# Performance work log

Measured on AMD Instinct MI355X. Metric: run time of the kernel, lower is better.

The kernel has to match this reference:

```python
import jax, jax.numpy as jnp
import numpy as np

PLAYERS = 8
DMODEL = 256          # cfg.dmodel (per-embedding dim)
DK = 1024             # cfg.dk
WINDOW = 4096         # cfg.window == T here
A_SPACE = 64
DFULL = DMODEL * 2 * PLAYERS   # 4096, the concatenated model dim


def _positional_encoding(T, dmodel):
    # i = 1/10000^(2j/dmodel); pe[:, ::2]=sin(pos*i), pe[:, 1::2]=cos(pos*i)
    i = 1.0 / jnp.power(jnp.float32(10000.0), jnp.arange(0, dmodel, 2, dtype=jnp.float32) / dmodel)
    pos = jnp.arange(T, dtype=jnp.float32)[:, None]
    pe = jnp.zeros((T, dmodel), dtype=jnp.float32)
    pe = pe.at[:, ::2].set(jnp.sin(pos * i))
    pe = pe.at[:, 1::2].set(jnp.cos(pos * i))
    return pe


def setup_inputs() -> dict:
    key = jax.random.key(0)
    ks = jax.random.split(key, 12)
    n_rows = WINDOW * 2 * PLAYERS  # 65536 one-hot rows
    idx = jax.random.randint(ks[0], (n_rows,), 0, PLAYERS + 1)
    obs = jax.nn.one_hot(idx, PLAYERS + 1, dtype=jnp.int32)
    std = 2.0 / (5.0 * DFULL)  # torch.normal(0, var) uses var as std in the source
    return {
        "obs": obs,
        "o_emb": jax.random.normal(ks[1], (PLAYERS + 1, DMODEL), jnp.float32),
        "d_emb": jax.random.normal(ks[2], (PLAYERS + 1, DMODEL), jnp.float32),
        "WQ": jax.random.normal(ks[3], (DFULL, DK), jnp.float32) * std,
        "WK": jax.random.normal(ks[4], (DFULL, DK), jnp.float32) * std,
        "WV": jax.random.normal(ks[5], (DFULL, DK), jnp.float32) * std,
        "WO": jax.random.normal(ks[6], (DK, DK), jnp.float32) * std,
        "Wo_pol": jax.random.normal(ks[7], (A_SPACE, DK), jnp.float32) * 0.02,
        "bo_pol": jnp.zeros((A_SPACE,), jnp.float32),
        "Wd_pol": jax.random.normal(ks[8], (A_SPACE, DK), jnp.float32) * 0.02,
        "bd_pol": jnp.zeros((A_SPACE,), jnp.float32),
        "Wv": jax.random.normal(ks[9], (1, DK), jnp.float32) * 0.02,
        "bv": jnp.zeros((1,), jnp.float32),
    }


def reference(obs, o_emb, d_emb, WQ, WK, WV, WO, Wo_pol, bo_pol, Wd_pol, bd_pol, Wv, bv):
    obs2 = obs.reshape(-1, PLAYERS + 1)
    # torch.where(row == 1)[1] on one-hot rows == argmax
    idx_o = jnp.argmax(obs2[::2], axis=1)   # [T*players]
    idx_d = jnp.argmax(obs2[1::2], axis=1)  # [T*players]
    emb = jnp.concatenate([o_emb[idx_o], d_emb[idx_d]], axis=1)  # [T*players, 2*dmodel]
    x = emb.reshape(-1, DFULL) * jnp.sqrt(jnp.float32(DMODEL))    # [T, DFULL]
    T = x.shape[0]
    x = x + _positional_encoding(T, DFULL)
    q = x @ WQ  # [T, DK]
    k = x @ WK
    v = x @ WV
    att = jax.nn.softmax((q @ k.T) / jnp.sqrt(jnp.float32(DK)), axis=-1)  # [T, T]
    o = (att @ v) @ WO  # [T, DK]
    h = jax.nn.relu(o[-1])  # last position only, [DK]
    o_logits = h @ Wo_pol.T + bo_pol  # [A_SPACE]
    d_logits = h @ Wd_pol.T + bd_pol  # [A_SPACE]
    value = h @ Wv.T + bv             # [1]
    return (o_logits, d_logits, value)
```

## Files before the change

### kernel.cpp

```cpp
#include <hip/hip_runtime.h>
#include <stdint.h>

#define DK      1024
#define NBLK    256
#define NT      1024
#define NBAR    5u
#define LOG2_10000 13.287712379549449f

__device__ __align__(16) float g_e[4096];
__device__ __align__(16) float g_kq[4096];
__device__ __align__(16) float g_ol[1024];
__device__ __align__(16) float g_q8[2][8][1024];
__device__ __align__(16) float g_ctx8[2][8][1024];
__device__ __align__(16) float g_w8[2][8][160];

__device__ unsigned bar_gc[256];
__device__ unsigned bar_gm[32];
__device__ unsigned bar_gen;

__device__ __forceinline__ void stg(float* p, float v) {
    __hip_atomic_store(p, v, __ATOMIC_RELAXED, __HIP_MEMORY_SCOPE_AGENT);
}
__device__ __forceinline__ float lda(const float* p) {
    return __hip_atomic_load(p, __ATOMIC_RELAXED, __HIP_MEMORY_SCOPE_AGENT);
}

__device__ __forceinline__ void gbar_arrive(int bid, unsigned target) {
    asm volatile("s_waitcnt vmcnt(0)" ::: "memory");
    __syncthreads();
    if (threadIdx.x == 0) {
        unsigned g = (unsigned)bid & 7u;
        unsigned old = __hip_atomic_fetch_add(&bar_gc[g * 32], 1u,
                           __ATOMIC_RELAXED, __HIP_MEMORY_SCOPE_AGENT);
        if (old == target * 32u - 1u) {
            unsigned o2 = __hip_atomic_fetch_add(&bar_gm[0], 1u,
                              __ATOMIC_RELAXED, __HIP_MEMORY_SCOPE_AGENT);
            if (o2 == target * 8u - 1u)
                __hip_atomic_store(&bar_gen, target, __ATOMIC_RELEASE,
                                   __HIP_MEMORY_SCOPE_AGENT);
        }
    }
}
__device__ __forceinline__ void gbar_wait(unsigned target) {
    if (threadIdx.x == 0) {
        int gd = 0;
        while (__hip_atomic_load(&bar_gen, __ATOMIC_RELAXED,
                                 __HIP_MEMORY_SCOPE_AGENT) < target) {
            __builtin_amdgcn_s_sleep(1);
            if (++gd > (1 << 17)) break;
        }
    }
    __syncthreads();
}
__device__ __forceinline__ void gbar(int bid, unsigned target) {
    gbar_arrive(bid, target);
    gbar_wait(target);
}

__device__ __forceinline__ float4 bred4(float4 a, float* buf, int tid) {
    #pragma unroll
    for (int off = 32; off; off >>= 1) {
        a.x += __shfl_down(a.x, off, 64);
        a.y += __shfl_down(a.y, off, 64);
        a.z += __shfl_down(a.z, off, 64);
        a.w += __shfl_down(a.w, off, 64);
    }
    float4* b4 = (float4*)buf;
    if ((tid & 63) == 0) b4[tid >> 6] = a;
    __syncthreads();
    float4 r = {0.f, 0.f, 0.f, 0.f};
    if (tid == 0) {
        #pragma unroll
        for (int i = 0; i < 16; ++i) {
            float4 t = b4[i];
            r.x += t.x; r.y += t.y; r.z += t.z; r.w += t.w;
        }
    }
    __syncthreads();
    return r;
}

__global__ __launch_bounds__(1024, 4) void fused_k(
        const int*   __restrict__ obs,
        const float* __restrict__ o_emb,  const float* __restrict__ d_emb,
        const float* __restrict__ WQ,     const float* __restrict__ WK,
        const float* __restrict__ WV,     const float* __restrict__ WO,
        const float* __restrict__ Wo_pol, const float* __restrict__ bo_pol,
        const float* __restrict__ Wd_pol, const float* __restrict__ bd_pol,
        const float* __restrict__ Wv,     const float* __restrict__ bv,
        float* __restrict__ out,          char* __restrict__ ws) {
    (void)ws;

    __shared__ __align__(16) float smem[12416];
    float* axpeL = &smem[12288];
    unsigned char* sidx = (unsigned char*)&smem[12304];
    unsigned* sgen = (unsigned*)&smem[12400];

    int bid = blockIdx.x, tid = threadIdx.x;
    const int w  = ((bid & 7) << 5) | (bid >> 3);
    const int sh = bid & 7;
    const int lane = tid & 63;
    const int ksub = tid >> 8, n4 = tid & 255;

    if (tid == 0)
        *sgen = __hip_atomic_load(&bar_gen, __ATOMIC_RELAXED,
                                  __HIP_MEMORY_SCOPE_AGENT);

    const float4* WQ4 = (const float4*)WQ;
    float4 wqr[4];
    #pragma unroll
    for (int kk = 0; kk < 4; ++kk)
        wqr[kk] = WQ4[(size_t)(w * 16 + ksub * 4 + kk) * 256 + n4];

    int*   lidx = (int*)&smem[4100];
    float* lx   = &smem[4120];
    if (tid < 256) {
        int g = w * 256 + tid;
        const int* r = obs + (size_t)g * 9;
        int id = 0;
        #pragma unroll
        for (int j = 1; j < 9; ++j) id += j * r[j];
        sidx[(tid & ~15) | ((tid & 1) << 3) | ((tid >> 1) & 7)] =
            (unsigned char)id;
    }
    if (tid < 16) {
        const int* rr = obs + (size_t)(65520 + tid) * 9;
        int id2 = 0;
        #pragma unroll
        for (int j = 1; j < 9; ++j) id2 += j * rr[j];
        lidx[(tid & 1) * 8 + (tid >> 1)] = id2;
    }
    __syncthreads();
    const unsigned gen0 = *sgen;
    const int par = (int)((gen0 / NBAR) & 1u);
    float* q8 = &g_q8[par][0][0];
    float* c8 = &g_ctx8[par][0][0];
    float* w8 = &g_w8[par][0][0];
    {
        float* q8n = &g_q8[par ^ 1][0][0];
        float* c8n = &g_ctx8[par ^ 1][0][0];
        float* w8n = &g_w8[par ^ 1][0][0];
        if (tid < 69) {
            int idx = w * 69 + tid;
            if (idx < 8192)       stg(&q8n[idx], 0.0f);
            else if (idx < 16384) stg(&c8n[idx - 8192], 0.0f);
            else if (idx < 17664) stg(&w8n[idx - 16384], 0.0f);
        }
    }
    if (tid < 16) {
        int c = w * 16 + tid;
        int p = c >> 9, rr = c & 511;
        const float* tab = (rr < 256) ? o_emb : d_emb;
        int slot = (rr < 256) ? p : 8 + p;
        int r2 = rr & 255;
        float e = tab[lidx[slot] * 256 + r2];
        float f = exp2f(-((float)(c & ~1) * (1.0f / 4096.0f)) * LOG2_10000);
        float sv, cv;
        __sincosf(4095.0f * f, &sv, &cv);
        lx[tid] = e * 16.0f + ((c & 1) ? cv : sv);
    }
    __syncthreads();
    {
        float4 acc = {0.f, 0.f, 0.f, 0.f};
        #pragma unroll
        for (int kk = 0; kk < 4; ++kk) {
            float xv = lx[ksub * 4 + kk];
            acc.x += xv * wqr[kk].x; acc.y += xv * wqr[kk].y;
            acc.z += xv * wqr[kk].z; acc.w += xv * wqr[kk].w;
        }
        float4* p4 = (float4*)smem;
        p4[ksub * 256 + n4] = acc;
        __syncthreads();
        if (tid < 256) {
            float4 a = p4[tid], b = p4[256 + tid],
                   c2 = p4[512 + tid], d = p4[768 + tid];
            float* dst = &q8[sh * 1024 + tid * 4];
            atomicAdd(dst + 0, a.x + b.x + c2.x + d.x);
            atomicAdd(dst + 1, a.y + b.y + c2.y + d.y);
            atomicAdd(dst + 2, a.z + b.z + c2.z + d.z);
            atomicAdd(dst + 3, a.w + b.w + c2.w + d.w);
        }
    }
    float4 wkr[4];
    gbar_arrive(bid, gen0 + 1);
    {
        const float4* WKr = (const float4*)(WK + (size_t)(w * 16 + (tid >> 6)) * DK);
        #pragma unroll
        for (int i = 0; i < 4; ++i) wkr[i] = WKr[i * 64 + lane];
        float* lemb = &smem[4096];
        float* lfrq = &smem[8724];
        for (int i = tid; i < 2048; i += NT)
            lfrq[i] = exp2f(-((float)(2 * i) * (1.0f / 4096.0f)) * LOG2_10000);
        for (int i = tid; i < 4608; i += NT) {
            int row = i >> 8, r = i & 255;
            lemb[row * 257 + r] = (row < 9) ? o_emb[row * 256 + r]
                                            : d_emb[(row - 9) * 256 + r];
        }
    }
    gbar_wait(gen0 + 1);

    {
        float* qsum = &smem[10772];
        float t = 0.0f;
        #pragma unroll
        for (int s2 = 0; s2 < 8; ++s2) t += lda(&q8[s2 * 1024 + tid]);
        qsum[tid] = t;
        __syncthreads();
        const float4* q4 = (const float4*)qsum;
        float acc = 0.0f;
        #pragma unroll
        for (int i = 0; i < 4; ++i) {
            float4 qq = q4[i * 64 + lane];
            acc += wkr[i].x * qq.x + wkr[i].y * qq.y
                 + wkr[i].z * qq.z + wkr[i].w * qq.w;
        }
        #pragma unroll
        for (int off = 32; off; off >>= 1) acc += __shfl_down(acc, off, 64);
        if (lane == 0) stg(&g_kq[w * 16 + (tid >> 6)], acc * (1.0f / 32.0f));
    }
    gbar(bid, gen0 + 2);

    {
        float* lkq   = smem;
        float* lemb  = &smem[4096];
        float* lfrq  = &smem[8724];
        float* ldot4 = &smem[10772];
        float* le16  = &smem[11360];
        float* lped  = &smem[11380];
        float* lh    = &smem[11400];
        #pragma unroll
        for (int i = 0; i < 4; ++i) {
            int c = tid + NT * i;
            lkq[c] = lda(&g_kq[c]);
        }
        if (tid < 144) lh[tid] = 0.0f;
        __syncthreads();
        if (tid < 576) {
            int p = tid >> 2, q = tid & 3;
            int sg = p / 9, id = p % 9;
            int base = (sg < 8) ? sg * 512 : (sg - 8) * 512 + 256;
            const float* e = lemb + ((sg < 8) ? id : (9 + id)) * 257;
            float a = 0.0f;
            for (int i = 0; i < 64; ++i) {
                int r = q * 64 + ((i + q * 13) & 63);
                a += e[r] * lkq[base + r];
            }
            ldot4[tid] = a;
        }
        {
            int tt = tid >> 6;
            int t = w * 16 + tt;
            float acc = 0.0f;
            #pragma unroll 4
            for (int jj = 0; jj < 32; ++jj) {
                int jf = jj * 64 + lane;
                float f = lfrq[jf];
                float svv, cvv;
                __sincosf((float)t * f, &svv, &cvv);
                acc += svv * lkq[2 * jf] + cvv * lkq[2 * jf + 1];
            }
            #pragma unroll
            for (int off = 32; off; off >>= 1) acc += __shfl_down(acc, off, 64);
            if (lane == 0) lped[tt] = acc;
        }
        __syncthreads();
        if (tid < 16) {
            float tot = lped[tid];
            const uint32_t* ip = (const uint32_t*)(sidx + tid * 16);
            uint32_t u0 = ip[0], u1 = ip[1], u2 = ip[2], u3 = ip[3];
            #pragma unroll
            for (int sg = 0; sg < 16; ++sg) {
                uint32_t u = (sg < 4) ? u0 : (sg < 8) ? u1 : (sg < 12) ? u2 : u3;
                int id = (u >> ((sg & 3) * 8)) & 0xFF;
                int p = (sg * 9 + id) * 4;
                tot += 16.0f * (ldot4[p] + ldot4[p + 1] + ldot4[p + 2] + ldot4[p + 3]);
            }
            float e = expf(tot);
            le16[tid] = e;
            stg(&g_e[w * 16 + tid], e);
        }
        __syncthreads();
        if (tid < 256) {
            int lt = tid >> 4, seg = tid & 15;
            int id = sidx[lt * 16 + seg];
            atomicAdd(&lh[seg * 9 + id], le16[lt]);
        }
        __syncthreads();
        if (tid < 144) atomicAdd(&w8[sh * 160 + tid], lh[tid]);
    }
    float4 wvr[4];
    gbar_arrive(bid, gen0 + 3);
    {
        const float4* WV4 = (const float4*)WV;
        #pragma unroll
        for (int kk = 0; kk < 4; ++kk)
            wvr[kk] = WV4[(size_t)(w * 16 + ksub * 4 + kk) * 256 + n4];
    }
    gbar_wait(gen0 + 3);

    {
        float* leT = smem;
        float* pss = &smem[4352];
        float* psc = &smem[5376];
        float* lw  = &smem[6400];
        float* axv = &smem[6576];
        {
            int c0 = tid * 4, col = tid >> 3;
            float e0 = lda(&g_e[c0 + 0]), e1 = lda(&g_e[c0 + 1]);
            float e2 = lda(&g_e[c0 + 2]), e3 = lda(&g_e[c0 + 3]);
            leT[((c0 + 0) & 31) * 129 + col] = e0;
            leT[((c0 + 1) & 31) * 129 + col] = e1;
            leT[((c0 + 2) & 31) * 129 + col] = e2;
            leT[((c0 + 3) & 31) * 129 + col] = e3;
        }
        if (tid < 144) {
            float s = 0.0f;
            #pragma unroll
            for (int s2 = 0; s2 < 8; ++s2) s += lda(&w8[s2 * 160 + tid]);
            lw[tid] = s;
        }
        __syncthreads();
        {
            int jl = tid >> 7, ts = tid & 127;
            int j = w * 8 + jl;
            float f = exp2f(-((float)(2 * j) * (1.0f / 4096.0f)) * LOG2_10000);
            float sf, cf;
            __sincosf(f, &sf, &cf);
            int t0 = ts * 32;
            float sv, cv;
            __sincosf((float)t0 * f, &sv, &cv);
            float ss = 0.f, sc = 0.f;
            #pragma unroll
            for (int i = 0; i < 32; ++i) {
                float a = leT[i * 129 + ts];
                ss += a * sv; sc += a * cv;
                float ns = sv * cf + cv * sf;
                cv = cv * cf - sv * sf;
                sv = ns;
            }
            pss[tid] = ss; psc[tid] = sc;
        }
        __syncthreads();
        if (tid < 512) {
            int m2 = tid >> 6, l = tid & 63;
            float a  = pss[m2 * 128 + l] + pss[m2 * 128 + 64 + l];
            float b2 = psc[m2 * 128 + l] + psc[m2 * 128 + 64 + l];
            #pragma unroll
            for (int off = 32; off; off >>= 1) {
                a  += __shfl_down(a, off, 64);
                b2 += __shfl_down(b2, off, 64);
            }
            if (l == 0) { axpeL[2 * m2] = a; axpeL[2 * m2 + 1] = b2; }
        }
        if (tid == 0) {
            float z = 0.0f;
            #pragma unroll
            for (int i = 0; i < 144; ++i) z += lw[i];
            smem[6560] = 16.0f / z;
        }
        __syncthreads();
        if (tid < 16) {
            int c = w * 16 + tid;
            int p = c >> 9, rr = c & 511;
            const float* tab = (rr < 256) ? o_emb : d_emb;
            int slot = (rr < 256) ? p : 8 + p;
            int r2 = rr & 255;
            float a = 0.0f;
            #pragma unroll
            for (int id2 = 0; id2 < 9; ++id2)
                a += lw[slot * 9 + id2] * tab[id2 * 256 + r2];
            axv[tid] = axpeL[tid] + 16.0f * a;
        }
        __syncthreads();
        {
            float4 acc = {0.f, 0.f, 0.f, 0.f};
            #pragma unroll
            for (int kk = 0; kk < 4; ++kk) {
                float av = axv[ksub * 4 + kk];
                acc.x += av * wvr[kk].x; acc.y += av * wvr[kk].y;
                acc.z += av * wvr[kk].z; acc.w += av * wvr[kk].w;
            }
            float4* p4 = (float4*)smem;
            p4[ksub * 256 + n4] = acc;
            __syncthreads();
            if (tid < 256) {
                float iz = smem[6560];
                float4 a = p4[tid], b = p4[256 + tid],
                       c2 = p4[512 + tid], d = p4[768 + tid];
                float* dst = &c8[sh * 1024 + tid * 4];
                atomicAdd(dst + 0, (a.x + b.x + c2.x + d.x) * iz);
                atomicAdd(dst + 1, (a.y + b.y + c2.y + d.y) * iz);
                atomicAdd(dst + 2, (a.z + b.z + c2.z + d.z) * iz);
                atomicAdd(dst + 3, (a.w + b.w + c2.w + d.w) * iz);
            }
        }
    }
    float4 wo;
    gbar_arrive(bid, gen0 + 4);
    wo = ((const float4*)WO)[(size_t)tid * 256 + w];
    gbar_wait(gen0 + 4);

    {
        float cj = 0.0f;
        #pragma unroll
        for (int s2 = 0; s2 < 8; ++s2) cj += lda(&c8[s2 * 1024 + tid]);
        float4 acc = {cj * wo.x, cj * wo.y, cj * wo.z, cj * wo.w};
        float4 s4 = bred4(acc, &smem[1024], tid);
        if (tid == 0) {
            stg(&g_ol[w * 4 + 0], s4.x); stg(&g_ol[w * 4 + 1], s4.y);
            stg(&g_ol[w * 4 + 2], s4.z); stg(&g_ol[w * 4 + 3], s4.w);
        }
    }
    float wvh = 0.0f, bh = 0.0f;
    gbar_arrive(bid, gen0 + 5);
    if (w < 129) {
        const float* Wh;
        if (w < 64)       { Wh = Wo_pol + (size_t)w * DK;        bh = bo_pol[w]; }
        else if (w < 128) { Wh = Wd_pol + (size_t)(w - 64) * DK; bh = bd_pol[w - 64]; }
        else              { Wh = Wv;                              bh = bv[0]; }
        wvh = Wh[tid];
    }
    gbar_wait(gen0 + 5);

    if (w < 129) {
        float sacc = fmaxf(lda(&g_ol[tid]), 0.0f) * wvh;
        #pragma unroll
        for (int off = 32; off; off >>= 1) sacc += __shfl_down(sacc, off, 64);
        float* red = smem;
        if ((tid & 63) == 0) red[tid >> 6] = sacc;
        __syncthreads();
        if (tid == 0) {
            float tot = bh;
            #pragma unroll
            for (int i = 0; i < 16; ++i) tot += red[i];
            out[w] = tot;
        }
    }
}

extern "C" void kernel_launch(void* const* d_in, const int* in_sizes, int n_in,
                              void* d_out, int out_size, void* d_ws, size_t ws_size,
                              hipStream_t stream) {
    const int*   obs    = (const int*)  d_in[0];
    const float* o_emb  = (const float*)d_in[1];
    const float* d_emb  = (const float*)d_in[2];
    const float* WQ     = (const float*)d_in[3];
    const float* WK     = (const float*)d_in[4];
    const float* WV     = (const float*)d_in[5];
    const float* WO     = (const float*)d_in[6];
    const float* Wo_pol = (const float*)d_in[7];
    const float* bo_pol = (const float*)d_in[8];
    const float* Wd_pol = (const float*)d_in[9];
    const float* bd_pol = (const float*)d_in[10];
    const float* Wv     = (const float*)d_in[11];
    const float* bv     = (const float*)d_in[12];
    float* out = (float*)d_out;
    char* ws   = (char*)d_ws;

    fused_k<<<dim3(NBLK), dim3(NT), 0, stream>>>(
        obs, o_emb, d_emb, WQ, WK, WV, WO,
        Wo_pol, bo_pol, Wd_pol, bd_pol, Wv, bv, out, ws);
}
```

Measured before the change: 148.8 us.

## Replace atomic-counter grid barrier with per-block flag slots and group leaders

The grid barrier no longer uses fetch_add counters. Each block now writes its target generation into its own slot. Eight leader blocks poll the 32 slots of their group and publish a group flag, and all blocks poll the eight group flags. This is meant to remove atomic contention and the serialized two-level counter chain. Separately, the one-hot index decoding is moved from before the first phase into the barrier-overlap window. The new barrier adds polling traffic and relies on relaxed loads without explicit acquire ordering, which adds a memory-ordering risk.

New measurement: 153.3 us. 3.0% more time.

```diff
diff --git a/kernel.cpp b/kernel.cpp
--- a/kernel.cpp
+++ b/kernel.cpp
@@ -14,38 +14,52 @@
 __device__ __align__(16) float g_ctx8[2][8][1024];
 __device__ __align__(16) float g_w8[2][8][160];
 
-__device__ unsigned bar_gc[256];
-__device__ unsigned bar_gm[32];
-__device__ unsigned bar_gen;
+__device__ unsigned bar_slot[8][32];
+__device__ unsigned bar_grpf[128];
 
 __device__ __forceinline__ void stg(float* p, float v) {
     __hip_atomic_store(p, v, __ATOMIC_RELAXED, __HIP_MEMORY_SCOPE_AGENT);
 }
+__device__ __forceinline__ void stgu(unsigned* p, unsigned v) {
+    __hip_atomic_store(p, v, __ATOMIC_RELAXED, __HIP_MEMORY_SCOPE_AGENT);
+}
 __device__ __forceinline__ float lda(const float* p) {
     return __hip_atomic_load(p, __ATOMIC_RELAXED, __HIP_MEMORY_SCOPE_AGENT);
 }
+__device__ __forceinline__ unsigned ldau(const unsigned* p) {
+    return __hip_atomic_load(p, __ATOMIC_RELAXED, __HIP_MEMORY_SCOPE_AGENT);
+}
 
 __device__ __forceinline__ void gbar_arrive(int bid, unsigned target) {
     asm volatile("s_waitcnt vmcnt(0)" ::: "memory");
     __syncthreads();
+    if (threadIdx.x == 0)
+        stgu(&bar_slot[bid & 7][bid >> 3], target);
+}
+__device__ __forceinline__ void gbar_wait(int bid, unsigned target) {
     if (threadIdx.x == 0) {
-        unsigned g = (unsigned)bid & 7u;
-        unsigned old = __hip_atomic_fetch_add(&bar_gc[g * 32], 1u,
-                           __ATOMIC_RELAXED, __HIP_MEMORY_SCOPE_AGENT);
-        if (old == target * 32u - 1u) {
-            unsigned o2 = __hip_atomic_fetch_add(&bar_gm[0], 1u,
-                              __ATOMIC_RELAXED, __HIP_MEMORY_SCOPE_AGENT);
-            if (o2 == target * 8u - 1u)
-                __hip_atomic_store(&bar_gen, target, __ATOMIC_RELEASE,
-                                   __HIP_MEMORY_SCOPE_AGENT);
-        }
-    }
-}
-__device__ __forceinline__ void gbar_wait(unsigned target) {
-    if (threadIdx.x == 0) {
+        if (bid < 8) {
+            int gd = 0;
+            for (;;) {
+                unsigned v[32], ok = 1u;
+                #pragma unroll
+                for (int i = 0; i < 32; ++i) v[i] = ldau(&bar_slot[bid][i]);
+                #pragma unroll
+                for (int i = 0; i < 32; ++i) ok &= (v[i] >= target) ? 1u : 0u;
+                if (ok) break;
+                __builtin_amdgcn_s_sleep(1);
+                if (++gd > (1 << 17)) break;
+            }
+            stgu(&bar_grpf[bid * 16], target);
+        }
         int gd = 0;
-        while (__hip_atomic_load(&bar_gen, __ATOMIC_RELAXED,
-                                 __HIP_MEMORY_SCOPE_AGENT) < target) {
+        for (;;) {
+            unsigned v[8], ok = 1u;
+            #pragma unroll
+            for (int g = 0; g < 8; ++g) v[g] = ldau(&bar_grpf[g * 16]);
+            #pragma unroll
+            for (int g = 0; g < 8; ++g) ok &= (v[g] >= target) ? 1u : 0u;
+            if (ok) break;
             __builtin_amdgcn_s_sleep(1);
             if (++gd > (1 << 17)) break;
         }
@@ -54,7 +68,7 @@
 }
 __device__ __forceinline__ void gbar(int bid, unsigned target) {
     gbar_arrive(bid, target);
-    gbar_wait(target);
+    gbar_wait(bid, target);
 }
 
 __device__ __forceinline__ float4 bred4(float4 a, float* buf, int tid) {
@@ -103,8 +117,7 @@
     const int ksub = tid >> 8, n4 = tid & 255;
 
     if (tid == 0)
-        *sgen = __hip_atomic_load(&bar_gen, __ATOMIC_RELAXED,
-                                  __HIP_MEMORY_SCOPE_AGENT);
+        *sgen = ldau(&bar_slot[bid & 7][bid >> 3]);
 
     const float4* WQ4 = (const float4*)WQ;
     float4 wqr[4];
@@ -114,15 +127,6 @@
 
     int*   lidx = (int*)&smem[4100];
     float* lx   = &smem[4120];
-    if (tid < 256) {
-        int g = w * 256 + tid;
-        const int* r = obs + (size_t)g * 9;
-        int id = 0;
-        #pragma unroll
-        for (int j = 1; j < 9; ++j) id += j * r[j];
-        sidx[(tid & ~15) | ((tid & 1) << 3) | ((tid >> 1) & 7)] =
-            (unsigned char)id;
-    }
     if (tid < 16) {
         const int* rr = obs + (size_t)(65520 + tid) * 9;
         int id2 = 0;
@@ -187,6 +191,15 @@
         const float4* WKr = (const float4*)(WK + (size_t)(w * 16 + (tid >> 6)) * DK);
         #pragma unroll
         for (int i = 0; i < 4; ++i) wkr[i] = WKr[i * 64 + lane];
+        if (tid < 256) {
+            int g = w * 256 + tid;
+            const int* r = obs + (size_t)g * 9;
+            int id = 0;
+            #pragma unroll
+            for (int j = 1; j < 9; ++j) id += j * r[j];
+            sidx[(tid & ~15) | ((tid & 1) << 3) | ((tid >> 1) & 7)] =
+                (unsigned char)id;
+        }
         float* lemb = &smem[4096];
         float* lfrq = &smem[8724];
         for (int i = tid; i < 2048; i += NT)
@@ -197,7 +210,7 @@
                                             : d_emb[(row - 9) * 256 + r];
         }
     }
-    gbar_wait(gen0 + 1);
+    gbar_wait(bid, gen0 + 1);
 
     {
         float* qsum = &smem[10772];
@@ -296,7 +309,7 @@
         for (int kk = 0; kk < 4; ++kk)
             wvr[kk] = WV4[(size_t)(w * 16 + ksub * 4 + kk) * 256 + n4];
     }
-    gbar_wait(gen0 + 3);
+    gbar_wait(bid, gen0 + 3);
 
     {
         float* leT = smem;
@@ -398,7 +411,7 @@
     float4 wo;
     gbar_arrive(bid, gen0 + 4);
     wo = ((const float4*)WO)[(size_t)tid * 256 + w];
-    gbar_wait(gen0 + 4);
+    gbar_wait(bid, gen0 + 4);
 
     {
         float cj = 0.0f;
@@ -420,7 +433,7 @@
         else              { Wh = Wv;                              bh = bv[0]; }
         wvh = Wh[tid];
     }
-    gbar_wait(gen0 + 5);
+    gbar_wait(bid, gen0 + 5);
 
     if (w < 129) {
         float sacc = fmaxf(lda(&g_ol[tid]), 0.0f) * wvh;
```
